# Kernel tuning notes

Measured on AMD Instinct MI355X. Metric: run time of the kernel, lower is better.

The kernel has to match this reference:

```python
import jax, jax.numpy as jnp
import numpy as np
from jax import lax

B, T, I, H, L, O = 256, 512, 64, 256, 2, 1


def _lstm_dir(x, w_ih, w_hh, b_ih, b_hh, reverse):
    # x: [B,T,Din]; w_ih: [4H,Din]; w_hh: [4H,H]; biases: [4H]
    Bn = x.shape[0]
    Hn = w_hh.shape[1]
    # precompute input projection for all timesteps
    xp = jnp.einsum('btd,gd->btg', x, w_ih) + b_ih + b_hh  # [B,T,4H]
    xp = jnp.swapaxes(xp, 0, 1)  # [T,B,4H]
    h0 = jnp.zeros((Bn, Hn), x.dtype)
    c0 = jnp.zeros((Bn, Hn), x.dtype)

    def step(carry, g_t):
        h, c = carry
        gates = g_t + h @ w_hh.T  # [B,4H]
        i, f, g, o = jnp.split(gates, 4, axis=-1)  # PyTorch gate order
        c = jax.nn.sigmoid(f) * c + jax.nn.sigmoid(i) * jnp.tanh(g)
        h = jax.nn.sigmoid(o) * jnp.tanh(c)
        return (h, c), h

    _, hs = lax.scan(step, (h0, c0), xp, reverse=reverse)  # hs: [T,B,H], time-aligned
    return jnp.swapaxes(hs, 0, 1)  # [B,T,H]


def setup_inputs() -> dict:
    key = jax.random.key(0)
    ks = jax.random.split(key, 20)
    s = 1.0 / np.sqrt(H)
    u = lambda k, shp: jax.random.uniform(k, shp, jnp.float32, -s, s)
    d = {
        'x': jax.random.normal(ks[0], (B, T, I), jnp.float32),
        # layer 0, forward and reverse directions
        'w_ih_l0': u(ks[1], (4 * H, I)), 'w_hh_l0': u(ks[2], (4 * H, H)),
        'b_ih_l0': u(ks[3], (4 * H,)), 'b_hh_l0': u(ks[4], (4 * H,)),
        'w_ih_l0r': u(ks[5], (4 * H, I)), 'w_hh_l0r': u(ks[6], (4 * H, H)),
        'b_ih_l0r': u(ks[7], (4 * H,)), 'b_hh_l0r': u(ks[8], (4 * H,)),
        # layer 1 (input dim = 2H from bidirectional concat)
        'w_ih_l1': u(ks[9], (4 * H, 2 * H)), 'w_hh_l1': u(ks[10], (4 * H, H)),
        'b_ih_l1': u(ks[11], (4 * H,)), 'b_hh_l1': u(ks[12], (4 * H,)),
        'w_ih_l1r': u(ks[13], (4 * H, 2 * H)), 'w_hh_l1r': u(ks[14], (4 * H, H)),
        'b_ih_l1r': u(ks[15], (4 * H,)), 'b_hh_l1r': u(ks[16], (4 * H,)),
        # fc head
        'fc_w': u(ks[17], (O, 2 * H)), 'fc_b': u(ks[18], (O,)),
    }
    return d


def reference(x, w_ih_l0, w_hh_l0, b_ih_l0, b_hh_l0,
              w_ih_l0r, w_hh_l0r, b_ih_l0r, b_hh_l0r,
              w_ih_l1, w_hh_l1, b_ih_l1, b_hh_l1,
              w_ih_l1r, w_hh_l1r, b_ih_l1r, b_hh_l1r,
              fc_w, fc_b):
    # layer 0
    h_fwd = _lstm_dir(x, w_ih_l0, w_hh_l0, b_ih_l0, b_hh_l0, reverse=False)
    h_bwd = _lstm_dir(x, w_ih_l0r, w_hh_l0r, b_ih_l0r, b_hh_l0r, reverse=True)
    h = jnp.concatenate([h_fwd, h_bwd], axis=-1)  # [B,T,2H]
    # layer 1
    h_fwd = _lstm_dir(h, w_ih_l1, w_hh_l1, b_ih_l1, b_hh_l1, reverse=False)
    h_bwd = _lstm_dir(h, w_ih_l1r, w_hh_l1r, b_ih_l1r, b_hh_l1r, reverse=True)
    h = jnp.concatenate([h_fwd, h_bwd], axis=-1)  # [B,T,2H]
    # fc on last timestep
    return h[:, -1, :] @ fc_w.T + fc_b  # [B,O]
```

## Files before the change

kernel.cpp:

```cpp
#include <hip/hip_runtime.h>

typedef __bf16 bf16_t;
typedef bf16_t bf16x8 __attribute__((ext_vector_type(8)));
typedef bf16_t bf16x4 __attribute__((ext_vector_type(4)));
typedef float f32x4 __attribute__((ext_vector_type(4)));

#define B_SZ 256
#define T_SZ 512
#define H_SZ 256
#define SCOPE_AGENT __HIP_MEMORY_SCOPE_AGENT
#define SENT32 0x7FC17FC1u

__device__ __forceinline__ float sigm(float x) { return 1.f / (1.f + __expf(-x)); }
__device__ __forceinline__ float tanhx(float x) {
  x = fminf(fmaxf(x, -15.f), 15.f);
  float e = __expf(-2.f * x);
  return (1.f - e) / (1.f + e);
}
__device__ __forceinline__ uint32_t pack_bf16x2(float a, float b) {
  union { bf16_t h[2]; uint32_t u; } v;
  v.h[0] = (bf16_t)a; v.h[1] = (bf16_t)b; return v.u;
}
__device__ __forceinline__ void st32_agent(uint32_t* p, uint32_t v) {
  __hip_atomic_store(p, v, __ATOMIC_RELAXED, SCOPE_AGENT);
}
__device__ __forceinline__ uint64_t ld64_agent(const uint64_t* p) {
  return __hip_atomic_load(p, __ATOMIC_RELAXED, SCOPE_AGENT);
}
__device__ __forceinline__ bool okv(uint64_t v) {
  return ((uint32_t)v != SENT32) & ((uint32_t)(v >> 32) != SENT32);
}
#define MFMA(a, b, c) __builtin_amdgcn_mfma_f32_16x16x32_bf16((a), (b), (c), 0, 0, 0)

__global__ __launch_bounds__(512, 2) void l0_scan(
    const bf16_t* __restrict__ xbf,
    const bf16_t* __restrict__ wih_f, const bf16_t* __restrict__ whhhi_f,
    const bf16_t* __restrict__ whhlo_f, const float* __restrict__ bias_f,
    const bf16_t* __restrict__ wih_b, const bf16_t* __restrict__ whhhi_b,
    const bf16_t* __restrict__ whhlo_b, const float* __restrict__ bias_b,
    bf16_t* __restrict__ h0) {
  const int id = blockIdx.x;
  const int ct = id >> 5;
  const int g  = id & 31;
  const int dir = g >> 4, bt = g & 15;
  const bf16_t* __restrict__ wih  = dir ? wih_b : wih_f;
  const bf16_t* __restrict__ whhh = dir ? whhhi_b : whhhi_f;
  const bf16_t* __restrict__ whhl = dir ? whhlo_b : whhlo_f;
  const float*  __restrict__ bias = dir ? bias_b : bias_f;

  const int tid = threadIdx.x;
  const int lane = tid & 63, wv = tid >> 6, l15 = lane & 15, quad = lane >> 4;
  const int b0 = bt * 16;

  __shared__ bf16_t hbl[16][264];
  __shared__ float  gl[16][260];

  bf16x8 wfi[2][2], wfh[2][8], wfl[2][8];
#pragma unroll
  for (int p = 0; p < 2; ++p) {
    const int gc = (wv * 2 + p) * 16 + l15;
    const int row = (gc >> 6) * H_SZ + ct * 64 + (gc & 63);
#pragma unroll
    for (int kt = 0; kt < 2; ++kt)
      wfi[p][kt] = *(const bf16x8*)(wih + (size_t)row * 64 + kt * 32 + quad * 8);
#pragma unroll
    for (int kt = 0; kt < 8; ++kt) {
      wfh[p][kt] = *(const bf16x8*)(whhh + (size_t)row * H_SZ + kt * 32 + quad * 8);
      wfl[p][kt] = *(const bf16x8*)(whhl + (size_t)row * H_SZ + kt * 32 + quad * 8);
    }
  }
  const int erow = tid >> 5, ecol = 2 * (tid & 31);
  const int gj = ct * 64 + ecol;
  float bia[4][2];
#pragma unroll
  for (int gg = 0; gg < 4; ++gg) {
    bia[gg][0] = bias[gg * H_SZ + gj];
    bia[gg][1] = bias[gg * H_SZ + gj + 1];
  }
  float2 c2 = {0.f, 0.f};
  const bf16_t* xrow = xbf + (size_t)(b0 + l15) * T_SZ * 64;
  const int prow = tid >> 5, pcq = (tid & 31) * 2;
  const bool own = ((tid & 31) >> 3) == ct;

  for (int s = 0; s < T_SZ; ++s) {
    const int t = dir ? (T_SZ - 1 - s) : s;
    f32x4 acc0 = {0.f, 0.f, 0.f, 0.f}, acc1 = {0.f, 0.f, 0.f, 0.f};
#pragma unroll
    for (int kt = 0; kt < 2; ++kt) {
      bf16x8 xa = *(const bf16x8*)(xrow + t * 64 + kt * 32 + quad * 8);
      acc0 = MFMA(xa, wfi[0][kt], acc0);
      acc1 = MFMA(xa, wfi[1][kt], acc1);
    }
    if (s == 0) {
      for (int i = tid; i < 16 * 264 / 2; i += 512) ((uint32_t*)hbl)[i] = 0u;
    } else if (!own) {
      const int tp = dir ? (t + 1) : (t - 1);
      const uint64_t* src =
          (const uint64_t*)(h0 + ((size_t)tp * B_SZ + b0 + prow) * 512 + dir * H_SZ) + pcq;
      uint64_t v0, v1;
      for (;;) {
        v0 = ld64_agent(src); v1 = ld64_agent(src + 1);
        if (okv(v0) && okv(v1)) break;
      }
      uint64_t* dst = (uint64_t*)&hbl[prow][pcq * 4];
      dst[0] = v0; dst[1] = v1;
    }
    __syncthreads();
#pragma unroll
    for (int kt = 0; kt < 8; ++kt) {
      bf16x8 ha = *(const bf16x8*)&hbl[l15][kt * 32 + quad * 8];
      acc0 = MFMA(ha, wfh[0][kt], acc0);
      acc0 = MFMA(ha, wfl[0][kt], acc0);
      acc1 = MFMA(ha, wfh[1][kt], acc1);
      acc1 = MFMA(ha, wfl[1][kt], acc1);
    }
#pragma unroll
    for (int r = 0; r < 4; ++r) {
      gl[quad * 4 + r][(wv * 2 + 0) * 16 + l15] = acc0[r];
      gl[quad * 4 + r][(wv * 2 + 1) * 16 + l15] = acc1[r];
    }
    __syncthreads();
    {
      float hv[2];
#pragma unroll
      for (int u = 0; u < 2; ++u) {
        float iv = sigm(gl[erow][0 * 64 + ecol + u] + bia[0][u]);
        float fv = sigm(gl[erow][1 * 64 + ecol + u] + bia[1][u]);
        float gv = tanhx(gl[erow][2 * 64 + ecol + u] + bia[2][u]);
        float ov = sigm(gl[erow][3 * 64 + ecol + u] + bia[3][u]);
        float cp = u ? c2.y : c2.x;
        float cn = fv * cp + iv * gv;
        if (u) c2.y = cn; else c2.x = cn;
        hv[u] = ov * tanhx(cn);
      }
      uint32_t pk = pack_bf16x2(hv[0], hv[1]);
      st32_agent((uint32_t*)(h0 + ((size_t)t * B_SZ + b0 + erow) * 512 + dir * H_SZ + gj),
                 pk);
      *(uint32_t*)&hbl[erow][gj] = pk;
    }
  }
}

__global__ __launch_bounds__(512, 2) void l1_scan(
    const bf16_t* __restrict__ h0,
    const bf16_t* __restrict__ wih, const bf16_t* __restrict__ whhh,
    const bf16_t* __restrict__ whhl, const float* __restrict__ bias,
    bf16_t* __restrict__ h1f, bf16_t* __restrict__ hg1) {
  const int id = blockIdx.x;
  const int ct = id >> 4, bt = id & 15;
  bf16_t* hgs = hg1 + (size_t)bt * T_SZ * 4096;

  const int tid = threadIdx.x;
  const int lane = tid & 63, wv = tid >> 6, l15 = lane & 15, quad = lane >> 4;
  const int b0 = bt * 16;

  __shared__ bf16_t ibl[2][16][520];
  __shared__ bf16_t hbl[16][264];
  __shared__ float  gl[16][132];

  const int gc = wv * 16 + l15;
  const int row = (gc >> 5) * H_SZ + ct * 32 + (gc & 31);
  bf16x8 wfi[16], wfh[8], wfl[8];
#pragma unroll
  for (int kt = 0; kt < 16; ++kt)
    wfi[kt] = *(const bf16x8*)(wih + (size_t)row * 512 + kt * 32 + quad * 8);
#pragma unroll
  for (int kt = 0; kt < 8; ++kt) {
    wfh[kt] = *(const bf16x8*)(whhh + (size_t)row * H_SZ + kt * 32 + quad * 8);
    wfl[kt] = *(const bf16x8*)(whhl + (size_t)row * H_SZ + kt * 32 + quad * 8);
  }
  const int et = tid & 255;
  const int erow = et >> 4, ecol = 2 * (et & 15);
  const int gj = ct * 32 + ecol;
  float bia[4][2];
#pragma unroll
  for (int g = 0; g < 4; ++g) {
    bia[g][0] = bias[g * H_SZ + gj];
    bia[g][1] = bias[g * H_SZ + gj + 1];
  }
  float2 c2 = {0.f, 0.f};
  const int prow = tid >> 5, pcq = (tid & 31) * 2;
  const bool own = ((tid & 31) >> 2) == ct;
  const int fr = tid >> 5, fcc = (tid & 31) * 16;

  {
    const bf16_t* src = h0 + ((size_t)(b0 + fr)) * 512 + fcc;
    *(bf16x8*)&ibl[0][fr][fcc]     = *(const bf16x8*)(src);
    *(bf16x8*)&ibl[0][fr][fcc + 8] = *(const bf16x8*)(src + 8);
  }
  __syncthreads();

  for (int s = 0; s < T_SZ; ++s) {
    const int cur = s & 1, nxt = cur ^ 1;
    bf16x8 pf0, pf1;
    if (s + 1 < T_SZ) {
      const bf16_t* src = h0 + ((size_t)(s + 1) * B_SZ + b0 + fr) * 512 + fcc;
      pf0 = *(const bf16x8*)(src);
      pf1 = *(const bf16x8*)(src + 8);
    }
    f32x4 acc = {0.f, 0.f, 0.f, 0.f};
#pragma unroll
    for (int kt = 0; kt < 16; ++kt) {
      bf16x8 a = *(const bf16x8*)&ibl[cur][l15][kt * 32 + quad * 8];
      acc = MFMA(a, wfi[kt], acc);
    }
    if (s == 0) {
      for (int i = tid; i < 16 * 264 / 2; i += 512) ((uint32_t*)hbl)[i] = 0u;
    } else if (!own) {
      const uint64_t* src =
          (const uint64_t*)(hgs + (size_t)(s - 1) * 4096 + prow * H_SZ) + pcq;
      uint64_t v0, v1;
      for (;;) {
        v0 = ld64_agent(src); v1 = ld64_agent(src + 1);
        if (okv(v0) && okv(v1)) break;
      }
      uint64_t* dst = (uint64_t*)&hbl[prow][pcq * 4];
      dst[0] = v0; dst[1] = v1;
    }
    if (s + 1 < T_SZ) {
      *(bf16x8*)&ibl[nxt][fr][fcc]     = pf0;
      *(bf16x8*)&ibl[nxt][fr][fcc + 8] = pf1;
    }
    __syncthreads();
#pragma unroll
    for (int kt = 0; kt < 8; ++kt) {
      bf16x8 ha = *(const bf16x8*)&hbl[l15][kt * 32 + quad * 8];
      acc = MFMA(ha, wfh[kt], acc);
      acc = MFMA(ha, wfl[kt], acc);
    }
#pragma unroll
    for (int r = 0; r < 4; ++r) gl[quad * 4 + r][wv * 16 + l15] = acc[r];
    __syncthreads();
    if (tid < 256) {
      float hv[2];
#pragma unroll
      for (int u = 0; u < 2; ++u) {
        float iv = sigm(gl[erow][0 * 32 + ecol + u] + bia[0][u]);
        float fv = sigm(gl[erow][1 * 32 + ecol + u] + bia[1][u]);
        float gv = tanhx(gl[erow][2 * 32 + ecol + u] + bia[2][u]);
        float ov = sigm(gl[erow][3 * 32 + ecol + u] + bia[3][u]);
        float cp = u ? c2.y : c2.x;
        float cn = fv * cp + iv * gv;
        if (u) c2.y = cn; else c2.x = cn;
        hv[u] = ov * tanhx(cn);
      }
      uint32_t pk = pack_bf16x2(hv[0], hv[1]);
      st32_agent((uint32_t*)(hgs + (size_t)s * 4096 + erow * H_SZ + gj), pk);
      *(uint32_t*)&hbl[erow][gj] = pk;
      if (s == T_SZ - 1)
        *(uint32_t*)(h1f + (size_t)(b0 + erow) * H_SZ + gj) = pk;
    }
  }
}

__global__ __launch_bounds__(256) void l1b_step(
    const bf16_t* __restrict__ h0, const bf16_t* __restrict__ wih_r,
    const float* __restrict__ bias_r, bf16_t* __restrict__ h1b) {
  const int bt = blockIdx.x >> 2, ct = blockIdx.x & 3;
  const int tid = threadIdx.x, lane = tid & 63, wv = tid >> 6;
  const int l15 = lane & 15, quad = lane >> 4;
  const int c0 = ct * 64 + wv * 16;
  const bf16_t* arow = h0 + ((size_t)(T_SZ - 1) * B_SZ + bt * 16 + l15) * 512;
  f32x4 acc[4] = {{0,0,0,0},{0,0,0,0},{0,0,0,0},{0,0,0,0}};
#pragma unroll 4
  for (int kt = 0; kt < 16; ++kt) {
    bf16x8 a = *(const bf16x8*)(arow + kt * 32 + quad * 8);
#pragma unroll
    for (int g = 0; g < 4; ++g) {
      bf16x8 w = *(const bf16x8*)(wih_r + (size_t)(g * H_SZ + c0 + l15) * 512 + kt * 32 + quad * 8);
      acc[g] = MFMA(a, w, acc[g]);
    }
  }
  const int j = c0 + l15;
  const float bi = bias_r[j], bg = bias_r[2 * H_SZ + j], bo = bias_r[3 * H_SZ + j];
#pragma unroll
  for (int r = 0; r < 4; ++r) {
    const int row = bt * 16 + quad * 4 + r;
    float iv = sigm(acc[0][r] + bi);
    float gv = tanhx(acc[2][r] + bg);
    float ov = sigm(acc[3][r] + bo);
    float cn = iv * gv;
    h1b[(size_t)row * H_SZ + j] = (bf16_t)(ov * tanhx(cn));
  }
}

__global__ void k_cvt4(const float* __restrict__ s, bf16_t* __restrict__ d, int n4) {
  int i = blockIdx.x * 256 + threadIdx.x;
  if (i < n4) {
    float4 v = ((const float4*)s)[i];
    bf16x4 o; o[0] = (bf16_t)v.x; o[1] = (bf16_t)v.y; o[2] = (bf16_t)v.z; o[3] = (bf16_t)v.w;
    ((bf16x4*)d)[i] = o;
  }
}
__global__ void k_split(const float* __restrict__ s, bf16_t* __restrict__ hi,
                        bf16_t* __restrict__ lo, int n) {
  int i = blockIdx.x * 256 + threadIdx.x;
  if (i < n) {
    float v = s[i];
    bf16_t h = (bf16_t)v;
    hi[i] = h;
    lo[i] = (bf16_t)(v - (float)h);
  }
}
__global__ void k_bias(const float* __restrict__ a, const float* __restrict__ b,
                       float* __restrict__ d, int n) {
  int i = blockIdx.x * 256 + threadIdx.x;
  if (i < n) d[i] = a[i] + b[i];
}
__global__ void k_fill4(uint4* __restrict__ p, int n) {
  int i = blockIdx.x * 256 + threadIdx.x;
  if (i < n) p[i] = make_uint4(SENT32, SENT32, SENT32, SENT32);
}
__global__ void k_fc(const bf16_t* __restrict__ hf, const bf16_t* __restrict__ hb,
                     const float* __restrict__ fw, const float* __restrict__ fb,
                     float* __restrict__ out) {
  int b = threadIdx.x;
  float s = fb[0];
  const bf16_t* pf = hf + (size_t)b * H_SZ;
  const bf16_t* pb = hb + (size_t)b * H_SZ;
  for (int j = 0; j < H_SZ; ++j) s += fw[j] * (float)pf[j];
  for (int j = 0; j < H_SZ; ++j) s += fw[H_SZ + j] * (float)pb[j];
  out[b] = s;
}

extern "C" void kernel_launch(void* const* d_in, const int* in_sizes, int n_in,
                              void* d_out, int out_size, void* d_ws, size_t ws_size,
                              hipStream_t stream) {
  (void)in_sizes; (void)n_in; (void)out_size; (void)ws_size;
  const float* x      = (const float*)d_in[0];
  const float* wih[4] = {(const float*)d_in[1], (const float*)d_in[5],
                         (const float*)d_in[9], (const float*)d_in[13]};
  const float* whh[4] = {(const float*)d_in[2], (const float*)d_in[6],
                         (const float*)d_in[10], (const float*)d_in[14]};
  const float* bih[4] = {(const float*)d_in[3], (const float*)d_in[7],
                         (const float*)d_in[11], (const float*)d_in[15]};
  const float* bhh[4] = {(const float*)d_in[4], (const float*)d_in[8],
                         (const float*)d_in[12], (const float*)d_in[16]};
  const float* fcw = (const float*)d_in[17];
  const float* fcb = (const float*)d_in[18];
  float* out = (float*)d_out;

  char* p = (char*)d_ws;
  auto take = [&](size_t bytes) { char* r = p; p += (bytes + 255) & ~(size_t)255; return r; };
  const int KinL[4] = {64, 64, 512, 512};
  bf16_t* wihb[4]; float* biasc[4]; bf16_t* whhhi[3]; bf16_t* whhlo[3];
  for (int k = 0; k < 4; ++k) {
    wihb[k]  = (bf16_t*)take((size_t)1024 * KinL[k] * 2);
    biasc[k] = (float*)take(1024 * 4);
  }
  for (int k = 0; k < 3; ++k) {
    whhhi[k] = (bf16_t*)take((size_t)1024 * 256 * 2);
    whhlo[k] = (bf16_t*)take((size_t)1024 * 256 * 2);
  }
  bf16_t* xbf = (bf16_t*)take((size_t)B_SZ * T_SZ * 64 * 2);
  bf16_t* h1f = (bf16_t*)take((size_t)B_SZ * H_SZ * 2);
  bf16_t* h1b = (bf16_t*)take((size_t)B_SZ * H_SZ * 2);
  char* sbeg = p;
  bf16_t* h0  = (bf16_t*)take((size_t)T_SZ * B_SZ * 512 * 2);
  bf16_t* hg1 = (bf16_t*)take((size_t)16 * T_SZ * 4096 * 2);
  size_t sbytes = (size_t)(p - sbeg);

  k_cvt4<<<dim3(8192), 256, 0, stream>>>(x, xbf, (B_SZ * T_SZ * 64) / 4);
  for (int k = 0; k < 4; ++k) {
    k_cvt4<<<dim3((1024 * KinL[k] / 4 + 255) / 256), 256, 0, stream>>>(
        wih[k], wihb[k], 1024 * KinL[k] / 4);
    k_bias<<<dim3(4), 256, 0, stream>>>(bih[k], bhh[k], biasc[k], 1024);
  }
  for (int k = 0; k < 3; ++k)
    k_split<<<dim3(1024), 256, 0, stream>>>(whh[k], whhhi[k], whhlo[k], 1024 * 256);
  {
    int n4 = (int)(sbytes / 16);
    k_fill4<<<dim3((n4 + 255) / 256), 256, 0, stream>>>((uint4*)sbeg, n4);
  }

  l0_scan<<<dim3(128), 512, 0, stream>>>(
      xbf, wihb[0], whhhi[0], whhlo[0], biasc[0],
           wihb[1], whhhi[1], whhlo[1], biasc[1], h0);
  l1_scan<<<dim3(128), 512, 0, stream>>>(
      h0, wihb[2], whhhi[2], whhlo[2], biasc[2], h1f, hg1);
  l1b_step<<<dim3(64), 256, 0, stream>>>(h0, wihb[3], biasc[3], h1b);

  k_fc<<<dim3(1), 256, 0, stream>>>(h1f, h1b, fcw, fcb, out);
}
```

Measured before the change: 2.110 ms.

## Restructure layer-0 scan so each wave owns all four gates, dropping LDS barriers

Each wave of the layer-0 recurrent kernel now computes all four gate columns for its 16 hidden units, so the LSTM cell update runs straight from the MFMA accumulators. This removes the shared-memory gate exchange and both per-step __syncthreads. Each lane also polls the previous hidden state directly from global memory into MFMA operands, including the block's own columns, instead of staging it in LDS. The block shrinks to 256 threads and per-thread register use roughly doubles, since each thread now holds four gates' worth of weight fragments. In exchange every lane issues more global polling loads per step.

Measured after the change: 3.310 ms. 56.9% more time.

```diff
diff --git a/kernel.cpp b/kernel.cpp
--- a/kernel.cpp
+++ b/kernel.cpp
@@ -21,6 +21,9 @@
   union { bf16_t h[2]; uint32_t u; } v;
   v.h[0] = (bf16_t)a; v.h[1] = (bf16_t)b; return v.u;
 }
+__device__ __forceinline__ uint32_t bf16bits(float a) {
+  union { bf16_t h; uint16_t u; } v; v.h = (bf16_t)a; return (uint32_t)v.u;
+}
 __device__ __forceinline__ void st32_agent(uint32_t* p, uint32_t v) {
   __hip_atomic_store(p, v, __ATOMIC_RELAXED, SCOPE_AGENT);
 }
@@ -32,7 +35,7 @@
 }
 #define MFMA(a, b, c) __builtin_amdgcn_mfma_f32_16x16x32_bf16((a), (b), (c), 0, 0, 0)
 
-__global__ __launch_bounds__(512, 2) void l0_scan(
+__global__ __launch_bounds__(256, 1) void l0_scan(
     const bf16_t* __restrict__ xbf,
     const bf16_t* __restrict__ wih_f, const bf16_t* __restrict__ whhhi_f,
     const bf16_t* __restrict__ whhlo_f, const float* __restrict__ bias_f,
@@ -51,92 +54,81 @@
   const int tid = threadIdx.x;
   const int lane = tid & 63, wv = tid >> 6, l15 = lane & 15, quad = lane >> 4;
   const int b0 = bt * 16;
-
-  __shared__ bf16_t hbl[16][264];
-  __shared__ float  gl[16][260];
-
-  bf16x8 wfi[2][2], wfh[2][8], wfl[2][8];
-#pragma unroll
-  for (int p = 0; p < 2; ++p) {
-    const int gc = (wv * 2 + p) * 16 + l15;
-    const int row = (gc >> 6) * H_SZ + ct * 64 + (gc & 63);
+  const int jc = ct * 64 + wv * 16 + l15;
+
+  bf16x8 wfi[4][2], wfh[4][8], wfl[4][8];
+#pragma unroll
+  for (int g4 = 0; g4 < 4; ++g4) {
+    const int row = g4 * H_SZ + jc;
 #pragma unroll
     for (int kt = 0; kt < 2; ++kt)
-      wfi[p][kt] = *(const bf16x8*)(wih + (size_t)row * 64 + kt * 32 + quad * 8);
+      wfi[g4][kt] = *(const bf16x8*)(wih + (size_t)row * 64 + kt * 32 + quad * 8);
 #pragma unroll
     for (int kt = 0; kt < 8; ++kt) {
-      wfh[p][kt] = *(const bf16x8*)(whhh + (size_t)row * H_SZ + kt * 32 + quad * 8);
-      wfl[p][kt] = *(const bf16x8*)(whhl + (size_t)row * H_SZ + kt * 32 + quad * 8);
-    }
-  }
-  const int erow = tid >> 5, ecol = 2 * (tid & 31);
-  const int gj = ct * 64 + ecol;
-  float bia[4][2];
-#pragma unroll
-  for (int gg = 0; gg < 4; ++gg) {
-    bia[gg][0] = bias[gg * H_SZ + gj];
-    bia[gg][1] = bias[gg * H_SZ + gj + 1];
-  }
-  float2 c2 = {0.f, 0.f};
+      wfh[g4][kt] = *(const bf16x8*)(whhh + (size_t)row * H_SZ + kt * 32 + quad * 8);
+      wfl[g4][kt] = *(const bf16x8*)(whhl + (size_t)row * H_SZ + kt * 32 + quad * 8);
+    }
+  }
+  float bia4[4];
+#pragma unroll
+  for (int g4 = 0; g4 < 4; ++g4) bia4[g4] = bias[g4 * H_SZ + jc];
+
+  f32x4 c4 = {0.f, 0.f, 0.f, 0.f};
   const bf16_t* xrow = xbf + (size_t)(b0 + l15) * T_SZ * 64;
-  const int prow = tid >> 5, pcq = (tid & 31) * 2;
-  const bool own = ((tid & 31) >> 3) == ct;
+  const int jc0 = ct * 64 + wv * 16 + (l15 & ~1);
+  const bool evn = (l15 & 1) == 0;
 
   for (int s = 0; s < T_SZ; ++s) {
     const int t = dir ? (T_SZ - 1 - s) : s;
-    f32x4 acc0 = {0.f, 0.f, 0.f, 0.f}, acc1 = {0.f, 0.f, 0.f, 0.f};
+    f32x4 acc[4] = {{0,0,0,0},{0,0,0,0},{0,0,0,0},{0,0,0,0}};
 #pragma unroll
     for (int kt = 0; kt < 2; ++kt) {
       bf16x8 xa = *(const bf16x8*)(xrow + t * 64 + kt * 32 + quad * 8);
-      acc0 = MFMA(xa, wfi[0][kt], acc0);
-      acc1 = MFMA(xa, wfi[1][kt], acc1);
-    }
-    if (s == 0) {
-      for (int i = tid; i < 16 * 264 / 2; i += 512) ((uint32_t*)hbl)[i] = 0u;
-    } else if (!own) {
+#pragma unroll
+      for (int g4 = 0; g4 < 4; ++g4) acc[g4] = MFMA(xa, wfi[g4][kt], acc[g4]);
+    }
+    if (s > 0) {
       const int tp = dir ? (t + 1) : (t - 1);
-      const uint64_t* src =
-          (const uint64_t*)(h0 + ((size_t)tp * B_SZ + b0 + prow) * 512 + dir * H_SZ) + pcq;
-      uint64_t v0, v1;
-      for (;;) {
-        v0 = ld64_agent(src); v1 = ld64_agent(src + 1);
-        if (okv(v0) && okv(v1)) break;
+      const uint64_t* hsrc =
+          (const uint64_t*)(h0 + ((size_t)tp * B_SZ + b0 + l15) * 512 + dir * H_SZ);
+      uint64_t v[16];
+      bool all;
+      do {
+        all = true;
+#pragma unroll
+        for (int kt = 0; kt < 8; ++kt) {
+          v[2 * kt]     = ld64_agent(hsrc + kt * 8 + quad * 2);
+          v[2 * kt + 1] = ld64_agent(hsrc + kt * 8 + quad * 2 + 1);
+          all = all && okv(v[2 * kt]) && okv(v[2 * kt + 1]);
+        }
+      } while (!all);
+#pragma unroll
+      for (int kt = 0; kt < 8; ++kt) {
+        union { uint64_t u[2]; bf16x8 h; } ha;
+        ha.u[0] = v[2 * kt]; ha.u[1] = v[2 * kt + 1];
+#pragma unroll
+        for (int g4 = 0; g4 < 4; ++g4) {
+          acc[g4] = MFMA(ha.h, wfh[g4][kt], acc[g4]);
+          acc[g4] = MFMA(ha.h, wfl[g4][kt], acc[g4]);
+        }
       }
-      uint64_t* dst = (uint64_t*)&hbl[prow][pcq * 4];
-      dst[0] = v0; dst[1] = v1;
-    }
-    __syncthreads();
-#pragma unroll
-    for (int kt = 0; kt < 8; ++kt) {
-      bf16x8 ha = *(const bf16x8*)&hbl[l15][kt * 32 + quad * 8];
-      acc0 = MFMA(ha, wfh[0][kt], acc0);
-      acc0 = MFMA(ha, wfl[0][kt], acc0);
-      acc1 = MFMA(ha, wfh[1][kt], acc1);
-      acc1 = MFMA(ha, wfl[1][kt], acc1);
     }
 #pragma unroll
     for (int r = 0; r < 4; ++r) {
-      gl[quad * 4 + r][(wv * 2 + 0) * 16 + l15] = acc0[r];
-      gl[quad * 4 + r][(wv * 2 + 1) * 16 + l15] = acc1[r];
-    }
-    __syncthreads();
-    {
-      float hv[2];
-#pragma unroll
-      for (int u = 0; u < 2; ++u) {
-        float iv = sigm(gl[erow][0 * 64 + ecol + u] + bia[0][u]);
-        float fv = sigm(gl[erow][1 * 64 + ecol + u] + bia[1][u]);
-        float gv = tanhx(gl[erow][2 * 64 + ecol + u] + bia[2][u]);
-        float ov = sigm(gl[erow][3 * 64 + ecol + u] + bia[3][u]);
-        float cp = u ? c2.y : c2.x;
-        float cn = fv * cp + iv * gv;
-        if (u) c2.y = cn; else c2.x = cn;
-        hv[u] = ov * tanhx(cn);
+      const int row = quad * 4 + r;
+      float iv = sigm(acc[0][r] + bia4[0]);
+      float fv = sigm(acc[1][r] + bia4[1]);
+      float gv = tanhx(acc[2][r] + bia4[2]);
+      float ov = sigm(acc[3][r] + bia4[3]);
+      float cn = fv * c4[r] + iv * gv;
+      c4[r] = cn;
+      uint32_t bits = bf16bits(ov * tanhx(cn));
+      uint32_t partner = (uint32_t)__shfl_xor((int)bits, 1);
+      if (evn) {
+        uint32_t pk = (bits & 0xffffu) | (partner << 16);
+        st32_agent((uint32_t*)(h0 + ((size_t)t * B_SZ + b0 + row) * 512 + dir * H_SZ + jc0),
+                   pk);
       }
-      uint32_t pk = pack_bf16x2(hv[0], hv[1]);
-      st32_agent((uint32_t*)(h0 + ((size_t)t * B_SZ + b0 + erow) * 512 + dir * H_SZ + gj),
-                 pk);
-      *(uint32_t*)&hbl[erow][gj] = pk;
     }
   }
 }
@@ -373,7 +365,7 @@
     k_fill4<<<dim3((n4 + 255) / 256), 256, 0, stream>>>((uint4*)sbeg, n4);
   }
 
-  l0_scan<<<dim3(128), 512, 0, stream>>>(
+  l0_scan<<<dim3(128), 256, 0, stream>>>(
       xbf, wihb[0], whhhi[0], whhlo[0], biasc[0],
            wihb[1], whhhi[1], whhlo[1], biasc[1], h0);
   l1_scan<<<dim3(128), 512, 0, stream>>>(
```
